# Performance work log

Measured on AMD Instinct MI355X. Metric: run time of the kernel, lower is better.

Reference implementation:

```python
import jax, jax.numpy as jnp
import numpy as np

EPSILON = 0.03   # entropic regularization
GAMMA = 0.5      # mass regularization
MAX_ITER = 10    # Sinkhorn iterations


def sinkhorn_unbalanced(feature1, feature2):
    # L2-normalize features
    f1 = feature1 / jnp.sqrt(jnp.sum(feature1 ** 2, -1, keepdims=True) + 1e-8)
    f2 = feature2 / jnp.sqrt(jnp.sum(feature2 ** 2, -1, keepdims=True) + 1e-8)
    C = 1.0 - jnp.einsum('bnc,bmc->bnm', f1, f2)       # cosine cost in [0, 2]
    K = jnp.exp(-C / EPSILON)                           # (B, N, M) Gibbs kernel
    B, N, M = K.shape
    power = GAMMA / (GAMMA + EPSILON)
    prob1 = jnp.full((B, N, 1), 1.0 / N, K.dtype)
    prob2 = jnp.full((B, M, 1), 1.0 / M, K.dtype)
    a = jnp.full((B, N, 1), 1.0 / N, K.dtype)
    b = jnp.full((B, M, 1), 1.0 / M, K.dtype)
    for _ in range(MAX_ITER):  # fixed small iteration count
        KTa = jnp.einsum('bnm,bno->bmo', K, a)
        b = (prob2 / (KTa + 1e-8)) ** power
        Kb = jnp.einsum('bnm,bmo->bno', K, b)
        a = (prob1 / (Kb + 1e-8)) ** power
    T = a * K * jnp.swapaxes(b, 1, 2)                   # transport plan (B, N, M)
    return T


def compute_rigid_transform(points1, points2, weights):
    # weighted SVD (Kabsch) on 3x3 covariances
    wn = weights[..., None] / (jnp.sum(weights[..., None], axis=1, keepdims=True) + 1e-5)
    centroid_a = jnp.sum(points1 * wn, axis=1)          # (B, 3)
    centroid_b = jnp.sum(points2 * wn, axis=1)
    a_c = points1 - centroid_a[:, None, :]
    b_c = points2 - centroid_b[:, None, :]
    cov = jnp.einsum('bnc,bnd->bcd', a_c, b_c * wn)     # (B, 3, 3)
    u, s, vh = jnp.linalg.svd(cov)
    v = jnp.swapaxes(vh, -1, -2)
    rot_pos = v @ jnp.swapaxes(u, -1, -2)
    v_neg = v.at[:, :, 2].multiply(-1.0)
    rot_neg = v_neg @ jnp.swapaxes(u, -1, -2)
    rot = jnp.where(jnp.linalg.det(rot_pos)[:, None, None] > 0, rot_pos, rot_neg)
    trans = -rot @ centroid_a[:, :, None] + centroid_b[:, :, None]
    return jnp.concatenate([rot, trans], axis=2)        # (B, 3, 4)


def setup_inputs() -> dict:
    key = jax.random.key(0)
    k1, k2, k3, k4 = jax.random.split(key, 4)
    B, N, M, C = 8, 4096, 4096, 256
    return {
        'feature1': jax.random.normal(k1, (B, N, C), jnp.float32),
        'feature2': jax.random.normal(k2, (B, M, C), jnp.float32),
        'points1': jax.random.normal(k3, (B, N, 3), jnp.float32),
        'points2': jax.random.normal(k4, (B, M, 3), jnp.float32),
    }


def reference(feature1, feature2, points1, points2):
    T = sinkhorn_unbalanced(feature1, feature2)          # (B, N, M)
    row_sum = jnp.sum(T, axis=-1, keepdims=True)         # (B, N, 1)
    corr = jnp.einsum('bnm,bmd->bnd', T, points2) / (row_sum + 1e-8)  # soft matches
    weights = jnp.squeeze(row_sum, -1)                   # (B, N)
    return compute_rigid_transform(points1, corr, weights)
```

## Files before the change

### kernel.cpp

```cpp
#include <hip/hip_runtime.h>

#define NB 8
#define NN 4096
#define MM 4096
#define CC 256

typedef unsigned short u16;
typedef __attribute__((ext_vector_type(4))) unsigned short u16x4;
typedef __attribute__((ext_vector_type(8))) short s16x8;
typedef __attribute__((ext_vector_type(4))) float f32x4;

#define INV_EPS 33.333333333333336f
#define EXP2_SCALE 48.089834696296504f
#define POWER   0.94339622641509435f
#define PROB    (1.0f/4096.0f)

static __device__ __forceinline__ float bf2f(u16 h) {
    union { unsigned int u; float f; } v;
    v.u = ((unsigned int)h) << 16;
    return v.f;
}
static __device__ __forceinline__ u16 f2bf(float f) {
    union { float f; unsigned int u; } v;
    v.f = f;
    unsigned int u = v.u;
    u += 0x7fffu + ((u >> 16) & 1u);
    return (u16)(u >> 16);
}
static __device__ __forceinline__ float gfun(float x) {
    return exp2f(POWER * log2f(PROB / (x + 1e-8f)));
}

__global__ __launch_bounds__(256) void norm_kernel(const float* __restrict__ src,
                                                   u16* __restrict__ dst)
{
    const int t = threadIdx.x, w = t >> 6, lane = t & 63;
    const size_t row = (size_t)blockIdx.x * 4 + w;
    const float* sp = src + row * CC + lane * 4;
    f32x4 v = *(const f32x4*)sp;
    float s = v.x * v.x + v.y * v.y + v.z * v.z + v.w * v.w;
    for (int o = 32; o > 0; o >>= 1) s += __shfl_xor(s, o);
    float rn = rsqrtf(s + 1e-8f);
    u16x4 o4;
    o4.x = f2bf(v.x * rn); o4.y = f2bf(v.y * rn);
    o4.z = f2bf(v.z * rn); o4.w = f2bf(v.w * rn);
    *(u16x4*)(dst + row * CC + lane * 4) = o4;
}

__global__ __launch_bounds__(256) void zero_kernel(float* __restrict__ KTa)
{
    KTa[blockIdx.x * 256 + threadIdx.x] = 0.f;
}

#define LDSS 72

__global__ __launch_bounds__(256, 3) void gemm_exp_kernel(
    const u16* __restrict__ f1s, const u16* __restrict__ f2s,
    u16* __restrict__ Ks, float* __restrict__ KTa)
{
    const int t = threadIdx.x;
    const int w = t >> 6, lane = t & 63;
    const int quad = lane >> 4, l15 = lane & 15;
    const int bx = blockIdx.x;
    const int by = blockIdx.y;
    const int ls = blockIdx.z;

    __shared__ u16 As[128 * LDSS];
    __shared__ u16 Bs[128 * LDSS];
    __shared__ float csum4[4][64];

    csum4[w][lane] = 0.f;

    const u16* f2base = f2s + ((size_t)ls * MM + (size_t)bx * 128) * CC;
    const u16* f1base = f1s + ((size_t)ls * NN + (size_t)by * 128) * CC;

    f32x4 acc[4][4];
#pragma unroll
    for (int i = 0; i < 4; ++i)
#pragma unroll
        for (int j = 0; j < 4; ++j) acc[i][j] = (f32x4){0.f, 0.f, 0.f, 0.f};

    const int g_r = t >> 3;
    const int g_c = (t & 7) << 3;

    for (int kt = 0; kt < 4; ++kt) {
        const int k0 = kt * 64;
        __syncthreads();
#pragma unroll
        for (int i = 0; i < 4; ++i) {
            const int row = g_r + i * 32;
            s16x8 va = *(const s16x8*)(f2base + (size_t)row * CC + k0 + g_c);
            s16x8 vb = *(const s16x8*)(f1base + (size_t)row * CC + k0 + g_c);
            *(s16x8*)&As[row * LDSS + g_c] = va;
            *(s16x8*)&Bs[row * LDSS + g_c] = vb;
        }
        __syncthreads();
#pragma unroll
        for (int s = 0; s < 2; ++s) {
            s16x8 af[4], bfr[4];
#pragma unroll
            for (int i = 0; i < 4; ++i)
                af[i] = *(const s16x8*)&As[((w & 1) * 64 + i * 16 + l15) * LDSS + s * 32 + quad * 8];
#pragma unroll
            for (int j = 0; j < 4; ++j)
                bfr[j] = *(const s16x8*)&Bs[((w >> 1) * 64 + j * 16 + l15) * LDSS + s * 32 + quad * 8];
#pragma unroll
            for (int i = 0; i < 4; ++i)
#pragma unroll
                for (int j = 0; j < 4; ++j)
                    acc[i][j] = __builtin_amdgcn_mfma_f32_16x16x32_bf16(af[i], bfr[j], acc[i][j], 0, 0, 0);
        }
    }

    u16* kb = Ks + (size_t)ls * NN * MM;
    const int rbase = by * 128 + (w >> 1) * 64 + l15;
    const int cbase = bx * 128 + (w & 1) * 64 + quad * 4;
    float part[4][4];
#pragma unroll
    for (int i = 0; i < 4; ++i)
#pragma unroll
        for (int e = 0; e < 4; ++e) part[i][e] = 0.f;

#pragma unroll
    for (int j = 0; j < 4; ++j) {
        const int r = rbase + j * 16;
#pragma unroll
        for (int i = 0; i < 4; ++i) {
            const int c = cbase + i * 16;
            f32x4 v = acc[i][j];
            const float e0 = exp2f((v.x - 1.f) * EXP2_SCALE);
            const float e1 = exp2f((v.y - 1.f) * EXP2_SCALE);
            const float e2 = exp2f((v.z - 1.f) * EXP2_SCALE);
            const float e3 = exp2f((v.w - 1.f) * EXP2_SCALE);
            u16x4 o;
            o.x = f2bf(e0); o.y = f2bf(e1); o.z = f2bf(e2); o.w = f2bf(e3);
            *(u16x4*)&kb[(size_t)r * MM + c] = o;
            part[i][0] += e0; part[i][1] += e1; part[i][2] += e2; part[i][3] += e3;
        }
    }

#pragma unroll
    for (int i = 0; i < 4; ++i)
#pragma unroll
        for (int e = 0; e < 4; ++e) {
            float v = part[i][e];
            v += __shfl_xor(v, 1); v += __shfl_xor(v, 2);
            v += __shfl_xor(v, 4); v += __shfl_xor(v, 8);
            if (l15 == 0)
                csum4[w][i * 16 + quad * 4 + e] += v;
        }
    __syncthreads();
    if (t < 128) {
        const int half = t >> 6, local = t & 63;
        const float v = csum4[half][local] + csum4[half + 2][local];
        atomicAdd(&KTa[(size_t)ls * MM + bx * 128 + t], v * PROB);
    }
}

__global__ __launch_bounds__(256) void bfin_kernel(float* __restrict__ KTa,
                                                   float* __restrict__ bvec)
{
    const int t = blockIdx.x * 256 + threadIdx.x;
    const float v = KTa[t];
    KTa[t] = 0.f;
    bvec[t] = gfun(v);
}

__global__ __launch_bounds__(256) void fused_kernel(const u16* __restrict__ Ks,
                                                    const float* __restrict__ bvec,
                                                    float* __restrict__ KTa)
{
    const int t = threadIdx.x, w = t >> 6, lane = t & 63;
    const int ls = blockIdx.x >> 7;
    const int chunk = blockIdx.x & 127;

    __shared__ float wp[2][4][4];
    __shared__ float kacc[4096];

    const float* bp = bvec + (size_t)ls * MM + t * 16;
    float bv[16];
#pragma unroll
    for (int i = 0; i < 4; ++i) {
        f32x4 b4 = *(const f32x4*)(bp + i * 4);
        bv[i * 4 + 0] = b4.x; bv[i * 4 + 1] = b4.y;
        bv[i * 4 + 2] = b4.z; bv[i * 4 + 3] = b4.w;
    }
    float acc[16];
#pragma unroll
    for (int i = 0; i < 16; ++i) acc[i] = 0.f;

    const u16* kbase = Ks + ((size_t)ls * NN + (size_t)chunk * 32) * MM + t * 16;

    for (int rb = 0; rb < 8; ++rb) {
        const u16* kp = kbase + (size_t)(rb * 4) * MM;
        const int par = rb & 1;

        s16x8 kv[4][2];
#pragma unroll
        for (int r = 0; r < 4; ++r) {
            kv[r][0] = *(const s16x8*)(kp + (size_t)r * MM);
            kv[r][1] = *(const s16x8*)(kp + (size_t)r * MM + 8);
        }
#pragma unroll
        for (int r = 0; r < 4; ++r) {
            const u16* u0 = (const u16*)&kv[r][0];
            const u16* u1 = (const u16*)&kv[r][1];
            float s = 0.f;
#pragma unroll
            for (int i = 0; i < 8; ++i) s += bf2f(u0[i]) * bv[i];
#pragma unroll
            for (int i = 0; i < 8; ++i) s += bf2f(u1[i]) * bv[8 + i];
            for (int o = 32; o > 0; o >>= 1) s += __shfl_xor(s, o);
            if (lane == 0) wp[par][r][w] = s;
        }
        __syncthreads();

        float ar[4];
#pragma unroll
        for (int r = 0; r < 4; ++r) {
            const float S = wp[par][r][0] + wp[par][r][1]
                          + wp[par][r][2] + wp[par][r][3];
            ar[r] = gfun(S);
        }

#pragma unroll
        for (int r = 0; r < 4; ++r) {
            const u16* u0 = (const u16*)&kv[r][0];
            const u16* u1 = (const u16*)&kv[r][1];
#pragma unroll
            for (int i = 0; i < 8; ++i) acc[i]     += ar[r] * bf2f(u0[i]);
#pragma unroll
            for (int i = 0; i < 8; ++i) acc[8 + i] += ar[r] * bf2f(u1[i]);
        }
    }

    __syncthreads();
#pragma unroll
    for (int i = 0; i < 4; ++i)
        *(f32x4*)&kacc[t * 16 + i * 4] =
            (f32x4){acc[i * 4 + 0], acc[i * 4 + 1], acc[i * 4 + 2], acc[i * 4 + 3]};
    __syncthreads();
    float* kout = KTa + (size_t)ls * MM;
#pragma unroll
    for (int i = 0; i < 16; ++i)
        atomicAdd(&kout[i * 256 + t], kacc[i * 256 + t]);
}

__global__ __launch_bounds__(256) void bp4_kernel(const float* __restrict__ bvec,
                                                  const float* __restrict__ p2,
                                                  float* __restrict__ bp4)
{
    const int t = blockIdx.x * 256 + threadIdx.x;
    const int ls = t >> 12;
    const int m = t & 4095;
    const float bv = bvec[t];
    const float x = p2[(size_t)t * 3 + 0];
    const float y = p2[(size_t)t * 3 + 1];
    const float z = p2[(size_t)t * 3 + 2];
    float* pb = bp4 + (size_t)ls * MM * 4;
    pb[m]          = bv;
    pb[MM + m]     = bv * x;
    pb[2 * MM + m] = bv * y;
    pb[3 * MM + m] = bv * z;
}

__global__ __launch_bounds__(256) void final_kernel(const u16* __restrict__ Ks,
                                                    const float* __restrict__ bp4,
                                                    float* __restrict__ wc4)
{
    __shared__ float planes[4][4096];
    const int t = threadIdx.x, w = t >> 6, lane = t & 63;
    const int ls = blockIdx.x >> 6;
    const int chunk = blockIdx.x & 63;

    const float* pb = bp4 + (size_t)ls * MM * 4;
#pragma unroll
    for (int p = 0; p < 4; ++p)
#pragma unroll
        for (int i = 0; i < 4; ++i) {
            const int idx = i * 1024 + t * 4;
            *(f32x4*)&planes[p][idx] = *(const f32x4*)(pb + p * MM + idx);
        }
    __syncthreads();

    for (int rr = 0; rr < 16; ++rr) {
        const int n = chunk * 64 + rr * 4 + w;
        const u16* kp = Ks + ((size_t)ls * NN + n) * MM;
        float s0 = 0.f, s1 = 0.f, s2 = 0.f, s3 = 0.f;
#pragma unroll 4
        for (int pass = 0; pass < 16; ++pass) {
            const int m = pass * 256 + lane * 4;
            u16x4 k4 = *(const u16x4*)(kp + m);
            f32x4 p0 = *(const f32x4*)&planes[0][m];
            f32x4 p1 = *(const f32x4*)&planes[1][m];
            f32x4 p2v = *(const f32x4*)&planes[2][m];
            f32x4 p3 = *(const f32x4*)&planes[3][m];
            const float k0 = bf2f(k4.x), k1 = bf2f(k4.y);
            const float k2 = bf2f(k4.z), k3 = bf2f(k4.w);
            s0 += k0 * p0.x + k1 * p0.y + k2 * p0.z + k3 * p0.w;
            s1 += k0 * p1.x + k1 * p1.y + k2 * p1.z + k3 * p1.w;
            s2 += k0 * p2v.x + k1 * p2v.y + k2 * p2v.z + k3 * p2v.w;
            s3 += k0 * p3.x + k1 * p3.y + k2 * p3.z + k3 * p3.w;
        }
        for (int o = 32; o > 0; o >>= 1) {
            s0 += __shfl_xor(s0, o); s1 += __shfl_xor(s1, o);
            s2 += __shfl_xor(s2, o); s3 += __shfl_xor(s3, o);
        }
        if (lane == 0) {
            const float av = gfun(s0);
            const float wgt = av * s0;
            const float inv = 1.f / (wgt + 1e-8f);
            f32x4 o = {av * s1 * inv, av * s2 * inv, av * s3 * inv, wgt};
            *(f32x4*)&wc4[((size_t)ls * NN + n) * 4] = o;
        }
    }
}

__global__ __launch_bounds__(256) void kabsch_kernel(const float* __restrict__ wc4,
                                                     const float* __restrict__ p1,
                                                     float* __restrict__ out)
{
    const int b = blockIdx.x;
    const int t = threadIdx.x, w = t >> 6, lane = t & 63;
    double acc[16];
#pragma unroll
    for (int k = 0; k < 16; ++k) acc[k] = 0.0;

    for (int n = t; n < NN; n += 256) {
        const float* wp = wc4 + ((size_t)b * NN + n) * 4;
        const float cx = wp[0], cy = wp[1], cz = wp[2], wgt = wp[3];
        const float* pp = p1 + ((size_t)b * NN + n) * 3;
        const double px = pp[0], py = pp[1], pz = pp[2];
        const double wd = wgt;
        const double wcx = wd * cx, wcy = wd * cy, wcz = wd * cz;
        acc[0] += wd;
        acc[1] += wd * px; acc[2] += wd * py; acc[3] += wd * pz;
        acc[4] += wcx;     acc[5] += wcy;     acc[6] += wcz;
        acc[7]  += px * wcx; acc[8]  += px * wcy; acc[9]  += px * wcz;
        acc[10] += py * wcx; acc[11] += py * wcy; acc[12] += py * wcz;
        acc[13] += pz * wcx; acc[14] += pz * wcy; acc[15] += pz * wcz;
    }

    __shared__ double red[4][16];
#pragma unroll
    for (int k = 0; k < 16; ++k) {
        double v = acc[k];
        for (int o = 32; o > 0; o >>= 1) v += __shfl_xor(v, o);
        acc[k] = v;
    }
    if (lane == 0)
        for (int k = 0; k < 16; ++k) red[w][k] = acc[k];
    __syncthreads();

    if (t == 0) {
        double S[16];
        for (int k = 0; k < 16; ++k)
            S[k] = red[0][k] + red[1][k] + red[2][k] + red[3][k];
        const double denom = S[0] + 1e-5;
        const double sfrac = S[0] / denom;
        double ca[3] = {S[1] / denom, S[2] / denom, S[3] / denom};
        double cb[3] = {S[4] / denom, S[5] / denom, S[6] / denom};
        double A[3][3], V[3][3];
        for (int i = 0; i < 3; ++i)
            for (int j = 0; j < 3; ++j) {
                A[i][j] = S[7 + i * 3 + j] / denom - (2.0 - sfrac) * ca[i] * cb[j];
                V[i][j] = (i == j) ? 1.0 : 0.0;
            }
        for (int sweep = 0; sweep < 20; ++sweep) {
            const int PP[3] = {0, 0, 1}, QQ[3] = {1, 2, 2};
            for (int r = 0; r < 3; ++r) {
                const int p = PP[r], q = QQ[r];
                double app = 0, aqq = 0, apq = 0;
                for (int i = 0; i < 3; ++i) {
                    app += A[i][p] * A[i][p];
                    aqq += A[i][q] * A[i][q];
                    apq += A[i][p] * A[i][q];
                }
                if (fabs(apq) < 1e-14 * (app + aqq) + 1e-300) continue;
                const double th = 0.5 * atan2(2.0 * apq, app - aqq);
                const double c = cos(th), sn = sin(th);
                for (int i = 0; i < 3; ++i) {
                    double x = A[i][p], y = A[i][q];
                    A[i][p] = c * x + sn * y; A[i][q] = -sn * x + c * y;
                    x = V[i][p]; y = V[i][q];
                    V[i][p] = c * x + sn * y; V[i][q] = -sn * x + c * y;
                }
            }
        }
        double sv[3];
        for (int j = 0; j < 3; ++j)
            sv[j] = sqrt(A[0][j] * A[0][j] + A[1][j] * A[1][j] + A[2][j] * A[2][j]);
        int idx[3] = {0, 1, 2};
        if (sv[idx[0]] < sv[idx[1]]) { int x = idx[0]; idx[0] = idx[1]; idx[1] = x; }
        if (sv[idx[0]] < sv[idx[2]]) { int x = idx[0]; idx[0] = idx[2]; idx[2] = x; }
        if (sv[idx[1]] < sv[idx[2]]) { int x = idx[1]; idx[1] = idx[2]; idx[2] = x; }
        double U[3][3], Vs[3][3];
        for (int j = 0; j < 3; ++j) {
            const int jj = idx[j];
            const double inv = 1.0 / fmax(sv[jj], 1e-300);
            for (int i = 0; i < 3; ++i) {
                U[i][j] = A[i][jj] * inv;
                Vs[i][j] = V[i][jj];
            }
        }
        double R[3][3];
        for (int i = 0; i < 3; ++i)
            for (int j = 0; j < 3; ++j)
                R[i][j] = Vs[i][0] * U[j][0] + Vs[i][1] * U[j][1] + Vs[i][2] * U[j][2];
        const double det = R[0][0] * (R[1][1] * R[2][2] - R[1][2] * R[2][1])
                         - R[0][1] * (R[1][0] * R[2][2] - R[1][2] * R[2][0])
                         + R[0][2] * (R[1][0] * R[2][1] - R[1][1] * R[2][0]);
        if (det < 0.0) {
            for (int i = 0; i < 3; ++i) Vs[i][2] = -Vs[i][2];
            for (int i = 0; i < 3; ++i)
                for (int j = 0; j < 3; ++j)
                    R[i][j] = Vs[i][0] * U[j][0] + Vs[i][1] * U[j][1] + Vs[i][2] * U[j][2];
        }
        double tr[3];
        for (int i = 0; i < 3; ++i)
            tr[i] = cb[i] - (R[i][0] * ca[0] + R[i][1] * ca[1] + R[i][2] * ca[2]);
        float* o = out + b * 12;
        for (int i = 0; i < 3; ++i) {
            o[i * 4 + 0] = (float)R[i][0];
            o[i * 4 + 1] = (float)R[i][1];
            o[i * 4 + 2] = (float)R[i][2];
            o[i * 4 + 3] = (float)tr[i];
        }
    }
}

extern "C" void kernel_launch(void* const* d_in, const int* in_sizes, int n_in,
                              void* d_out, int out_size, void* d_ws, size_t ws_size,
                              hipStream_t stream) {
    const float* f1 = (const float*)d_in[0];
    const float* f2 = (const float*)d_in[1];
    const float* p1 = (const float*)d_in[2];
    const float* p2 = (const float*)d_in[3];
    float* out = (float*)d_out;

    const size_t AL = 256;
    const size_t szK   = (size_t)NN * MM * 2;
    const size_t szF1  = (size_t)NN * CC * 2;
    const size_t szF2  = (size_t)MM * CC * 2;
    const size_t szB   = (size_t)MM * 4;
    const size_t szKTa = (size_t)MM * 4;
    const size_t szBp4 = (size_t)MM * 16;
    const size_t szWc4 = (size_t)NN * 16;
    const size_t per_batch = szK + szF1 + szF2 + szB + szKTa + szBp4 + szWc4 + 8 * AL;

    int NS = (int)(ws_size / per_batch);
    if (NS > NB) NS = NB;
    if (NS < 1) NS = 1;

    char* base = (char*)d_ws;
    size_t off = 0;
    auto carve = [&](size_t bytes) -> char* {
        char* p = base + off;
        off += (bytes + AL - 1) & ~(AL - 1);
        return p;
    };
    u16*   Ks   = (u16*)  carve((size_t)NS * szK);
    u16*   f1s  = (u16*)  carve((size_t)NS * szF1);
    u16*   f2s  = (u16*)  carve((size_t)NS * szF2);
    float* bvec = (float*)carve((size_t)NS * szB);
    float* KTa  = (float*)carve((size_t)NS * szKTa);
    float* bp4  = (float*)carve((size_t)NS * szBp4);
    float* wc4  = (float*)carve((size_t)NS * szWc4);

    for (int b0 = 0; b0 < NB; b0 += NS) {
        const int cnt = (NB - b0 < NS) ? (NB - b0) : NS;

        norm_kernel<<<cnt * NN / 4, 256, 0, stream>>>(f1 + (size_t)b0 * NN * CC, f1s);
        norm_kernel<<<cnt * MM / 4, 256, 0, stream>>>(f2 + (size_t)b0 * MM * CC, f2s);
        zero_kernel<<<cnt * MM / 256, 256, 0, stream>>>(KTa);
        gemm_exp_kernel<<<dim3(MM / 128, NN / 128, cnt), 256, 0, stream>>>(f1s, f2s, Ks, KTa);
        bfin_kernel<<<cnt * MM / 256, 256, 0, stream>>>(KTa, bvec);

        for (int it = 0; it < 9; ++it) {
            fused_kernel<<<cnt * 128, 256, 0, stream>>>(Ks, bvec, KTa);
            bfin_kernel<<<cnt * MM / 256, 256, 0, stream>>>(KTa, bvec);
        }

        bp4_kernel<<<cnt * MM / 256, 256, 0, stream>>>(bvec, p2 + (size_t)b0 * MM * 3, bp4);
        final_kernel<<<cnt * 64, 256, 0, stream>>>(Ks, bp4, wc4);
        kabsch_kernel<<<cnt, 256, 0, stream>>>(wc4, p1 + (size_t)b0 * NN * 3, out + (size_t)b0 * 12);
    }

    (void)in_sizes; (void)n_in; (void)out_size;
}
```

Before: 1.029 ms.

## Replace atomic column-sum accumulation with per-block partial buffers reduced in bfin

The GEMM-exp and Sinkhorn fused kernels now write per-block column partial sums into a partition buffer, replacing atomicAdd into a shared KTa vector. bfin_kernel then sums the partitions (32 or 128) per column before applying the power function. This removes atomic contention, the zero kernel and the LDS staging and syncs in fused_kernel, at the cost of extra memory traffic for the partial buffers and a serial loop in bfin. The change also shrinks the LDS padding from 72 to 68 and lowers the gemm launch-bounds occupancy hint from 3 to 2.

```diff
diff --git a/kernel.cpp b/kernel.cpp
--- a/kernel.cpp
+++ b/kernel.cpp
@@ -4,6 +4,7 @@
 #define NN 4096
 #define MM 4096
 #define CC 256
+#define NPART 128
 
 typedef unsigned short u16;
 typedef __attribute__((ext_vector_type(4))) unsigned short u16x4;
@@ -47,16 +48,11 @@
     *(u16x4*)(dst + row * CC + lane * 4) = o4;
 }
 
-__global__ __launch_bounds__(256) void zero_kernel(float* __restrict__ KTa)
-{
-    KTa[blockIdx.x * 256 + threadIdx.x] = 0.f;
-}
-
-#define LDSS 72
-
-__global__ __launch_bounds__(256, 3) void gemm_exp_kernel(
+#define LDSS 68
+
+__global__ __launch_bounds__(256, 2) void gemm_exp_kernel(
     const u16* __restrict__ f1s, const u16* __restrict__ f2s,
-    u16* __restrict__ Ks, float* __restrict__ KTa)
+    u16* __restrict__ Ks, float* __restrict__ part)
 {
     const int t = threadIdx.x;
     const int w = t >> 6, lane = t & 63;
@@ -115,11 +111,11 @@
     u16* kb = Ks + (size_t)ls * NN * MM;
     const int rbase = by * 128 + (w >> 1) * 64 + l15;
     const int cbase = bx * 128 + (w & 1) * 64 + quad * 4;
-    float part[4][4];
+    float partl[4][4];
 #pragma unroll
     for (int i = 0; i < 4; ++i)
 #pragma unroll
-        for (int e = 0; e < 4; ++e) part[i][e] = 0.f;
+        for (int e = 0; e < 4; ++e) partl[i][e] = 0.f;
 
 #pragma unroll
     for (int j = 0; j < 4; ++j) {
@@ -135,7 +131,7 @@
             u16x4 o;
             o.x = f2bf(e0); o.y = f2bf(e1); o.z = f2bf(e2); o.w = f2bf(e3);
             *(u16x4*)&kb[(size_t)r * MM + c] = o;
-            part[i][0] += e0; part[i][1] += e1; part[i][2] += e2; part[i][3] += e3;
+            partl[i][0] += e0; partl[i][1] += e1; partl[i][2] += e2; partl[i][3] += e3;
         }
     }
 
@@ -143,7 +139,7 @@
     for (int i = 0; i < 4; ++i)
 #pragma unroll
         for (int e = 0; e < 4; ++e) {
-            float v = part[i][e];
+            float v = partl[i][e];
             v += __shfl_xor(v, 1); v += __shfl_xor(v, 2);
             v += __shfl_xor(v, 4); v += __shfl_xor(v, 8);
             if (l15 == 0)
@@ -153,29 +149,31 @@
     if (t < 128) {
         const int half = t >> 6, local = t & 63;
         const float v = csum4[half][local] + csum4[half + 2][local];
-        atomicAdd(&KTa[(size_t)ls * MM + bx * 128 + t], v * PROB);
-    }
-}
-
-__global__ __launch_bounds__(256) void bfin_kernel(float* __restrict__ KTa,
-                                                   float* __restrict__ bvec)
-{
-    const int t = blockIdx.x * 256 + threadIdx.x;
-    const float v = KTa[t];
-    KTa[t] = 0.f;
-    bvec[t] = gfun(v);
+        part[((size_t)ls * NPART + by) * MM + bx * 128 + t] = v * PROB;
+    }
+}
+
+__global__ __launch_bounds__(256) void bfin_kernel(const float* __restrict__ part,
+                                                   float* __restrict__ bvec,
+                                                   int nparts)
+{
+    const int c = blockIdx.x * 256 + threadIdx.x;
+    const int ls = c >> 12, m = c & 4095;
+    const float* pp = part + (size_t)ls * NPART * MM + m;
+    float s = 0.f;
+    for (int p = 0; p < nparts; ++p) s += pp[(size_t)p * MM];
+    bvec[c] = gfun(s);
 }
 
 __global__ __launch_bounds__(256) void fused_kernel(const u16* __restrict__ Ks,
                                                     const float* __restrict__ bvec,
-                                                    float* __restrict__ KTa)
+                                                    float* __restrict__ part)
 {
     const int t = threadIdx.x, w = t >> 6, lane = t & 63;
     const int ls = blockIdx.x >> 7;
     const int chunk = blockIdx.x & 127;
 
     __shared__ float wp[2][4][4];
-    __shared__ float kacc[4096];
 
     const float* bp = bvec + (size_t)ls * MM + t * 16;
     float bv[16];
@@ -234,16 +232,11 @@
         }
     }
 
-    __syncthreads();
+    float* kout = part + ((size_t)ls * NPART + chunk) * MM + t * 16;
 #pragma unroll
     for (int i = 0; i < 4; ++i)
-        *(f32x4*)&kacc[t * 16 + i * 4] =
+        *(f32x4*)&kout[i * 4] =
             (f32x4){acc[i * 4 + 0], acc[i * 4 + 1], acc[i * 4 + 2], acc[i * 4 + 3]};
-    __syncthreads();
-    float* kout = KTa + (size_t)ls * MM;
-#pragma unroll
-    for (int i = 0; i < 16; ++i)
-        atomicAdd(&kout[i * 256 + t], kacc[i * 256 + t]);
 }
 
 __global__ __launch_bounds__(256) void bp4_kernel(const float* __restrict__ bvec,
@@ -439,14 +432,14 @@
     float* out = (float*)d_out;
 
     const size_t AL = 256;
-    const size_t szK   = (size_t)NN * MM * 2;
-    const size_t szF1  = (size_t)NN * CC * 2;
-    const size_t szF2  = (size_t)MM * CC * 2;
-    const size_t szB   = (size_t)MM * 4;
-    const size_t szKTa = (size_t)MM * 4;
-    const size_t szBp4 = (size_t)MM * 16;
-    const size_t szWc4 = (size_t)NN * 16;
-    const size_t per_batch = szK + szF1 + szF2 + szB + szKTa + szBp4 + szWc4 + 8 * AL;
+    const size_t szK    = (size_t)NN * MM * 2;
+    const size_t szF1   = (size_t)NN * CC * 2;
+    const size_t szF2   = (size_t)MM * CC * 2;
+    const size_t szB    = (size_t)MM * 4;
+    const size_t szPart = (size_t)NPART * MM * 4;
+    const size_t szBp4  = (size_t)MM * 16;
+    const size_t szWc4  = (size_t)NN * 16;
+    const size_t per_batch = szK + szF1 + szF2 + szB + szPart + szBp4 + szWc4 + 8 * AL;
 
     int NS = (int)(ws_size / per_batch);
     if (NS > NB) NS = NB;
@@ -463,7 +456,7 @@
     u16*   f1s  = (u16*)  carve((size_t)NS * szF1);
     u16*   f2s  = (u16*)  carve((size_t)NS * szF2);
     float* bvec = (float*)carve((size_t)NS * szB);
-    float* KTa  = (float*)carve((size_t)NS * szKTa);
+    float* part = (float*)carve((size_t)NS * szPart);
     float* bp4  = (float*)carve((size_t)NS * szBp4);
     float* wc4  = (float*)carve((size_t)NS * szWc4);
 
@@ -472,13 +465,12 @@
 
         norm_kernel<<<cnt * NN / 4, 256, 0, stream>>>(f1 + (size_t)b0 * NN * CC, f1s);
         norm_kernel<<<cnt * MM / 4, 256, 0, stream>>>(f2 + (size_t)b0 * MM * CC, f2s);
-        zero_kernel<<<cnt * MM / 256, 256, 0, stream>>>(KTa);
-        gemm_exp_kernel<<<dim3(MM / 128, NN / 128, cnt), 256, 0, stream>>>(f1s, f2s, Ks, KTa);
-        bfin_kernel<<<cnt * MM / 256, 256, 0, stream>>>(KTa, bvec);
+        gemm_exp_kernel<<<dim3(MM / 128, NN / 128, cnt), 256, 0, stream>>>(f1s, f2s, Ks, part);
+        bfin_kernel<<<cnt * MM / 256, 256, 0, stream>>>(part, bvec, 32);
 
         for (int it = 0; it < 9; ++it) {
-            fused_kernel<<<cnt * 128, 256, 0, stream>>>(Ks, bvec, KTa);
-            bfin_kernel<<<cnt * MM / 256, 256, 0, stream>>>(KTa, bvec);
+            fused_kernel<<<cnt * 128, 256, 0, stream>>>(Ks, bvec, part);
+            bfin_kernel<<<cnt * MM / 256, 256, 0, stream>>>(part, bvec, NPART);
         }
 
         bp4_kernel<<<cnt * MM / 256, 256, 0, stream>>>(bvec, p2 + (size_t)b0 * MM * 3, bp4);
```

Result: slower. 1.571 ms (+52.7%).
